# Optimization experiments

Hardware: AMD Instinct MI355X
Metric: run time of the kernel (lower is better)

The kernel has to match this reference:

```python
import jax, jax.numpy as jnp
import numpy as np

B, L, D = 32, 512, 384
T_MAX = 4096
PAD_VALUE = 0.0
EXPAND_SCALE = 1.0


def setup_inputs() -> dict:
    key = jax.random.key(0)
    k1, k2, k3 = jax.random.split(key, 3)
    sequence = jax.random.normal(k1, (B, L, D), dtype=jnp.float32)
    duration = jax.random.randint(k2, (B, L), 0, 8, dtype=jnp.int64)
    padding_mask = jax.random.randint(k3, (B, L), 0, 2) == 1
    return {"sequence": sequence, "duration": duration,
            "padding_mask": padding_mask, "max_length": T_MAX}


def reference(sequence, duration, padding_mask, max_length):
    # expanded_duration = round(expand_scale * duration)
    exp_dur = jnp.round(EXPAND_SCALE * duration.astype(jnp.float32)).astype(jnp.int32)
    # mask padded tokens in the input sequence with pad_value
    seq = jnp.where(padding_mask[..., None], PAD_VALUE, sequence)  # (B, L, D)
    # cumulative durations: token t occupies output slots [cum[t-1], cum[t])
    cum = jnp.cumsum(exp_dur, axis=1)  # (B, L)
    pos = jnp.arange(max_length, dtype=cum.dtype)  # (T,)
    # idx[b, j] = first token index whose cumulative end exceeds j
    idx = jax.vmap(lambda c: jnp.searchsorted(c, pos, side="right"))(cum)  # (B, T)
    valid = pos[None, :] < cum[:, -1:]  # (B, T): within total expanded length
    idx = jnp.clip(idx, 0, seq.shape[1] - 1)
    out = jnp.take_along_axis(seq, idx[..., None], axis=1)  # (B, T, D)
    out = jnp.where(valid[..., None], out, PAD_VALUE)
    return out, exp_dur
```

## Files before the change

kernel.cpp:

```cpp
#include <hip/hip_runtime.h>

constexpr int B = 32;
constexpr int L = 512;
constexpr int D = 384;
constexpr int T = 4096;
constexpr int VPR = D / 4;
constexpr int OUT0 = B * T * D;
constexpr int NROWS = B * T;
constexpr int TOTAL4 = NROWS * VPR;

__global__ void scan_k(const int* __restrict__ dur, int* __restrict__ cum,
                       float* __restrict__ exp_dur_out) {
    const int b = blockIdx.x;
    const int t = threadIdx.x;
    __shared__ int s[L];
    int d = dur[b * L + t];
    exp_dur_out[b * L + t] = (float)d;
    s[t] = d;
    __syncthreads();
    #pragma unroll
    for (int off = 1; off < L; off <<= 1) {
        int v = (t >= off) ? s[t - off] : 0;
        __syncthreads();
        s[t] += v;
        __syncthreads();
    }
    cum[b * L + t] = s[t];
}

__global__ void idx_k(const int* __restrict__ cum, const int* __restrict__ mask,
                      int* __restrict__ idxmap) {
    const int i = blockIdx.x * blockDim.x + threadIdx.x;
    if (i >= NROWS) return;
    const int b = i >> 12;
    const int j = i & (T - 1);
    const int* c = cum + b * L;
    const int total = c[L - 1];
    int res = -1;
    if (j < total) {
        int lo = 0, hi = L;
        while (lo < hi) {
            int mid = (lo + hi) >> 1;
            if (c[mid] <= j) lo = mid + 1; else hi = mid;
        }
        res = mask[b * L + lo] ? -1 : (b * L + lo);
    }
    idxmap[i] = res;
}

__global__ void gather_k(const float4* __restrict__ seq,
                         const int* __restrict__ idxmap,
                         float4* __restrict__ out) {
    const int i = blockIdx.x * blockDim.x + threadIdx.x;
    if (i >= TOTAL4) return;
    const int row = i / VPR;
    const int col = i - row * VPR;
    const int src = idxmap[row];
    float4 v = make_float4(0.f, 0.f, 0.f, 0.f);
    if (src >= 0) v = seq[src * VPR + col];
    out[i] = v;
}

extern "C" void kernel_launch(void* const* d_in, const int* in_sizes, int n_in,
                              void* d_out, int out_size, void* d_ws, size_t ws_size,
                              hipStream_t stream) {
    const float* seq  = (const float*)d_in[0];
    const int*   dur  = (const int*)d_in[1];
    const int*   mask = (const int*)d_in[2];

    float* out      = (float*)d_out;
    float* expd_out = out + OUT0;

    int* cum    = (int*)d_ws;
    int* idxmap = (int*)((char*)d_ws + B * L * 4);

    scan_k<<<B, L, 0, stream>>>(dur, cum, expd_out);

    {
        const int bs = 256;
        idx_k<<<(NROWS + bs - 1) / bs, bs, 0, stream>>>(cum, mask, idxmap);
    }
    {
        const int bs = 256;
        gather_k<<<(TOTAL4 + bs - 1) / bs, bs, 0, stream>>>(
            (const float4*)seq, idxmap, (float4*)out);
    }
}
```

Before: 233.3 us.

## Fuse index search and gather into one kernel with shared cumsum

```diff
diff --git a/kernel.cpp b/kernel.cpp
--- a/kernel.cpp
+++ b/kernel.cpp
@@ -6,11 +6,15 @@
 constexpr int T = 4096;
 constexpr int VPR = D / 4;
 constexpr int OUT0 = B * T * D;
-constexpr int NROWS = B * T;
-constexpr int TOTAL4 = NROWS * VPR;
+constexpr int RPB = 16;
+constexpr int BLOCKS_PER_BATCH = T / RPB;
+constexpr int NBLK = B * BLOCKS_PER_BATCH;
+constexpr int BS = 256;
+constexpr int PASSES = RPB * VPR / BS;
 
-__global__ void scan_k(const int* __restrict__ dur, int* __restrict__ cum,
-                       float* __restrict__ exp_dur_out) {
+__global__ __launch_bounds__(L) void scan_k(const int* __restrict__ dur,
+                                            int* __restrict__ cum,
+                                            float* __restrict__ exp_dur_out) {
     const int b = blockIdx.x;
     const int t = threadIdx.x;
     __shared__ int s[L];
@@ -28,37 +32,51 @@
     cum[b * L + t] = s[t];
 }
 
-__global__ void idx_k(const int* __restrict__ cum, const int* __restrict__ mask,
-                      int* __restrict__ idxmap) {
-    const int i = blockIdx.x * blockDim.x + threadIdx.x;
-    if (i >= NROWS) return;
-    const int b = i >> 12;
-    const int j = i & (T - 1);
-    const int* c = cum + b * L;
-    const int total = c[L - 1];
-    int res = -1;
-    if (j < total) {
-        int lo = 0, hi = L;
-        while (lo < hi) {
-            int mid = (lo + hi) >> 1;
-            if (c[mid] <= j) lo = mid + 1; else hi = mid;
+__global__ __launch_bounds__(BS) void fused_k(const float4* __restrict__ seq,
+                                              const int* __restrict__ cum,
+                                              const int* __restrict__ mask,
+                                              float4* __restrict__ out) {
+    __shared__ int s_cum[L];
+    __shared__ int s_src[RPB];
+
+    const int blk   = blockIdx.x;
+    const int b     = blk >> 8;
+    const int chunk = blk & 255;
+    const int row0  = chunk * RPB;
+    const int tid   = threadIdx.x;
+
+    #pragma unroll
+    for (int i = 0; i < L / BS; ++i)
+        s_cum[i * BS + tid] = cum[b * L + i * BS + tid];
+    __syncthreads();
+
+    if (tid < RPB) {
+        const int j = row0 + tid;
+        const int total = s_cum[L - 1];
+        int res = -1;
+        if (j < total) {
+            int lo = 0, hi = L;
+            while (lo < hi) {
+                int mid = (lo + hi) >> 1;
+                if (s_cum[mid] <= j) lo = mid + 1; else hi = mid;
+            }
+            res = mask[b * L + lo] ? -1 : (b * L + lo);
         }
-        res = mask[b * L + lo] ? -1 : (b * L + lo);
+        s_src[tid] = res;
     }
-    idxmap[i] = res;
-}
+    __syncthreads();
 
-__global__ void gather_k(const float4* __restrict__ seq,
-                         const int* __restrict__ idxmap,
-                         float4* __restrict__ out) {
-    const int i = blockIdx.x * blockDim.x + threadIdx.x;
-    if (i >= TOTAL4) return;
-    const int row = i / VPR;
-    const int col = i - row * VPR;
-    const int src = idxmap[row];
-    float4 v = make_float4(0.f, 0.f, 0.f, 0.f);
-    if (src >= 0) v = seq[src * VPR + col];
-    out[i] = v;
+    float4* obase = out + (size_t)(b * T + row0) * VPR;
+    #pragma unroll
+    for (int p = 0; p < PASSES; ++p) {
+        const int idx = p * BS + tid;
+        const int r   = idx / VPR;
+        const int col = idx - r * VPR;
+        const int s   = s_src[r];
+        float4 v = make_float4(0.f, 0.f, 0.f, 0.f);
+        if (s >= 0) v = seq[(size_t)s * VPR + col];
+        obase[idx] = v;
+    }
 }
 
 extern "C" void kernel_launch(void* const* d_in, const int* in_sizes, int n_in,
@@ -71,18 +89,9 @@
     float* out      = (float*)d_out;
     float* expd_out = out + OUT0;
 
-    int* cum    = (int*)d_ws;
-    int* idxmap = (int*)((char*)d_ws + B * L * 4);
+    int* cum = (int*)d_ws;
 
     scan_k<<<B, L, 0, stream>>>(dur, cum, expd_out);
-
-    {
-        const int bs = 256;
-        idx_k<<<(NROWS + bs - 1) / bs, bs, 0, stream>>>(cum, mask, idxmap);
-    }
-    {
-        const int bs = 256;
-        gather_k<<<(TOTAL4 + bs - 1) / bs, bs, 0, stream>>>(
-            (const float4*)seq, idxmap, (float4*)out);
-    }
+    fused_k<<<NBLK, BS, 0, stream>>>((const float4*)seq, cum, mask,
+                                     (float4*)out);
 }
```

Result: faster. 217.5 us (-6.8%).
